# Kernel tuning notes

Hardware: AMD Instinct MI355X
Metric: run time of the kernel (lower is better)

The kernel has to match this reference:

```python
import jax, jax.numpy as jnp
import numpy as np

N, E = 20000, 320000
IN_F, EF, H, C = 2, 1, 128, 2
BN_S = 1.0 / float(np.sqrt(1.0 + 1e-5))  # eval-mode BatchNorm1d with running mean 0, var 1


def _gated_gcn_conv(h, e, src, dst, p, act, residual):
    # DGL GatedGCNConv: e' = C e + D h_src + E h_dst;
    # h' = A h + sum_{in-edges} sigmoid(e') * B h_src / (sum sigmoid(e') + 1e-6)
    Aw, Ab, Bw, Bb, Cw, Cb, Dw, Db, Ew, Eb, bhg, bhb, beg, beb = p
    h_in, e_in = h, e
    Ah = h @ Aw + Ab
    Bh = h @ Bw + Bb
    Dh = h @ Dw + Db
    Eh = h @ Ew + Eb
    e2 = e @ Cw + Cb + Dh[src] + Eh[dst]          # [E, H]
    sig = jax.nn.sigmoid(e2)
    num = jax.ops.segment_sum(sig * Bh[src], dst, num_segments=N)  # [N, H]
    den = jax.ops.segment_sum(sig, dst, num_segments=N)            # [N, H]
    h2 = Ah + num / (den + 1e-6)
    # BatchNorm (eval): (x - 0)/sqrt(1 + eps) * gamma + beta
    h2 = bhg * (h2 * BN_S) + bhb
    e2 = beg * (e2 * BN_S) + beb
    h2, e2 = act(h2), act(e2)
    if residual:
        h2 = h2 + h_in
        e2 = e2 + e_in
    return h2, e2


def _forward(node_feats, edge_feats, src, dst, P):
    (a0_w, a0_b, b0_w, b0_b, c0_w, c0_b, d0_w, d0_b, e0_w, e0_b,
     bnh0_g, bnh0_b, bne0_g, bne0_b,
     aL_w, aL_b, bL_w, bL_b, cL_w, cL_b, dL_w, dL_b, eL_w, eL_b,
     bnhL_g, bnhL_b, bneL_g, bneL_b,
     mlp_w1, mlp_b1, mlp_w2, mlp_b2) = P
    h, e = node_feats, edge_feats
    # layer 0: elu inside conv, residual off (2->128, 1->128)
    p0 = (a0_w, a0_b, b0_w, b0_b, c0_w, c0_b, d0_w, d0_b, e0_w, e0_b,
          bnh0_g, bnh0_b, bne0_g, bne0_b)
    h, e = _gated_gcn_conv(h, e, src, dst, p0, jax.nn.elu, residual=False)
    h = jax.nn.leaky_relu(h)
    e = jax.nn.leaky_relu(e)
    # layers 1..2: leaky_relu inside conv, residual on (128->128)
    for l in range(2):
        pl = (aL_w[l], aL_b[l], bL_w[l], bL_b[l], cL_w[l], cL_b[l],
              dL_w[l], dL_b[l], eL_w[l], eL_b[l],
              bnhL_g[l], bnhL_b[l], bneL_g[l], bneL_b[l])
        h, e = _gated_gcn_conv(h, e, src, dst, pl, jax.nn.leaky_relu, residual=True)
        h = jax.nn.leaky_relu(h)
        e = jax.nn.leaky_relu(e)
    # edge classifier: gather endpoints, concat with edge feats, MLP
    edge_repr = jnp.concatenate([h[src], h[dst], e], axis=1)  # [E, 3H]
    hid = jax.nn.relu(edge_repr @ mlp_w1 + mlp_b1)
    return hid @ mlp_w2 + mlp_b2                               # [E, C]


PARAM_NAMES = ["a0_w", "a0_b", "b0_w", "b0_b", "c0_w", "c0_b", "d0_w", "d0_b",
               "e0_w", "e0_b", "bnh0_g", "bnh0_b", "bne0_g", "bne0_b",
               "aL_w", "aL_b", "bL_w", "bL_b", "cL_w", "cL_b", "dL_w", "dL_b",
               "eL_w", "eL_b", "bnhL_g", "bnhL_b", "bneL_g", "bneL_b",
               "mlp_w1", "mlp_b1", "mlp_w2", "mlp_b2"]


def setup_inputs() -> dict:
    key = jax.random.key(0)
    ks = iter(jax.random.split(key, 64))
    nrm = lambda shp: jax.random.normal(next(ks), shp, dtype=jnp.float32) * 0.05
    inp = {}
    inp["node_feats"] = jax.random.normal(next(ks), (N, IN_F), dtype=jnp.float32)
    inp["edge_feats"] = jax.random.normal(next(ks), (E, EF), dtype=jnp.float32)
    inp["src"] = jax.random.randint(next(ks), (E,), 0, N, dtype=jnp.int32)
    inp["dst"] = jax.random.randint(next(ks), (E,), 0, N, dtype=jnp.int32)
    # layer 0 linears (A,B,D,E: in->H; C: edge->H), biases zero-init like common practice
    for nm, din in [("a0", IN_F), ("b0", IN_F), ("c0", EF), ("d0", IN_F), ("e0", IN_F)]:
        inp[nm + "_w"] = nrm((din, H))
        inp[nm + "_b"] = nrm((H,))
    inp["bnh0_g"] = jnp.ones((H,), jnp.float32)
    inp["bnh0_b"] = jnp.zeros((H,), jnp.float32)
    inp["bne0_g"] = jnp.ones((H,), jnp.float32)
    inp["bne0_b"] = jnp.zeros((H,), jnp.float32)
    # layers 1..2 stacked
    for nm in ["aL", "bL", "cL", "dL", "eL"]:
        inp[nm + "_w"] = nrm((2, H, H))
        inp[nm + "_b"] = nrm((2, H))
    inp["bnhL_g"] = jnp.ones((2, H), jnp.float32)
    inp["bnhL_b"] = jnp.zeros((2, H), jnp.float32)
    inp["bneL_g"] = jnp.ones((2, H), jnp.float32)
    inp["bneL_b"] = jnp.zeros((2, H), jnp.float32)
    # edge MLP
    inp["mlp_w1"] = nrm((3 * H, H))
    inp["mlp_b1"] = nrm((H,))
    inp["mlp_w2"] = nrm((H, C))
    inp["mlp_b2"] = nrm((C,))
    return inp


def reference(node_feats, edge_feats, src, dst,
              a0_w, a0_b, b0_w, b0_b, c0_w, c0_b, d0_w, d0_b, e0_w, e0_b,
              bnh0_g, bnh0_b, bne0_g, bne0_b,
              aL_w, aL_b, bL_w, bL_b, cL_w, cL_b, dL_w, dL_b, eL_w, eL_b,
              bnhL_g, bnhL_b, bneL_g, bneL_b,
              mlp_w1, mlp_b1, mlp_w2, mlp_b2):
    P = (a0_w, a0_b, b0_w, b0_b, c0_w, c0_b, d0_w, d0_b, e0_w, e0_b,
         bnh0_g, bnh0_b, bne0_g, bne0_b,
         aL_w, aL_b, bL_w, bL_b, cL_w, cL_b, dL_w, dL_b, eL_w, eL_b,
         bnhL_g, bnhL_b, bneL_g, bneL_b,
         mlp_w1, mlp_b1, mlp_w2, mlp_b2)
    return _forward(node_feats, edge_feats, src, dst, P)
```

## Files before the change

### kernel.cpp

```cpp
#include <hip/hip_runtime.h>
#include <hip/hip_bf16.h>
#include <math.h>

#define NN 20000
#define NE 320000
#define H 128
#define NH (NN * H)

typedef short bf16x8 __attribute__((ext_vector_type(8)));
typedef float f32x4 __attribute__((ext_vector_type(4)));
typedef unsigned short u16x8 __attribute__((ext_vector_type(8)));

__device__ __forceinline__ float lrelu(float x) { return x > 0.f ? x : 0.01f * x; }
__device__ __forceinline__ float eluf(float x)  { return x > 0.f ? x : expm1f(x); }
__device__ __forceinline__ float sigf(float x)  { return 1.f / (1.f + __expf(-x)); }
__device__ __forceinline__ unsigned short f2b(float x) {
    __hip_bfloat16 h = __float2bfloat16(x);
    return *reinterpret_cast<unsigned short*>(&h);
}
__device__ __forceinline__ float b2f(unsigned short u) {
    __hip_bfloat16 h = *reinterpret_cast<__hip_bfloat16*>(&u);
    return __bfloat162float(h);
}
#define BN_S 0.99999500003749973f

struct PackPtrs { const float* w[13]; };
__global__ __launch_bounds__(256) void k_pack(PackPtrs p, unsigned short* __restrict__ dst) {
    int gid = blockIdx.x * 256 + threadIdx.x;
    int m = gid >> 11;
    int r = gid & 2047;
    int t = r >> 8, kk = (r >> 6) & 3, lane = r & 63;
    const float* W = p.w[m];
    int col = t * 16 + (lane & 15);
    int krow = kk * 32 + (lane >> 4) * 8;
    unsigned short* o = dst + (size_t)m * 16384 + (size_t)r * 8;
#pragma unroll
    for (int j = 0; j < 8; ++j) o[j] = f2b(W[(krow + j) * H + col]);
}

__global__ __launch_bounds__(256) void k_deg(const int* __restrict__ dst, int* __restrict__ deg) {
    int e = blockIdx.x * 256 + threadIdx.x;
    if (e < NE) atomicAdd(&deg[dst[e]], 1);
}

__global__ __launch_bounds__(256) void k_scan(const int* __restrict__ deg,
                                              int* __restrict__ off, int* __restrict__ cursor) {
    __shared__ int sums[256];
    const int t = threadIdx.x;
    const int per = (NN + 255) / 256;
    const int base = t * per;
    int s = 0;
    for (int i = 0; i < per; ++i) { int idx = base + i; if (idx < NN) s += deg[idx]; }
    sums[t] = s;
    __syncthreads();
    for (int d = 1; d < 256; d <<= 1) {
        int v = (t >= d) ? sums[t - d] : 0;
        __syncthreads();
        sums[t] += v;
        __syncthreads();
    }
    int run = (t == 0) ? 0 : sums[t - 1];
    for (int i = 0; i < per; ++i) {
        int idx = base + i;
        if (idx < NN) { off[idx] = run; cursor[idx] = run; run += deg[idx]; }
    }
}

__global__ __launch_bounds__(256) void k_fill(const int* __restrict__ dst,
                                              int* __restrict__ cursor, int* __restrict__ csr) {
    int e = blockIdx.x * 256 + threadIdx.x;
    if (e < NE) {
        int pos = atomicAdd(&cursor[dst[e]], 1);
        csr[pos] = e;
    }
}

__global__ __launch_bounds__(256) void k_seqs(const int* __restrict__ csr,
                                              const int* __restrict__ src,
                                              const int* __restrict__ dst,
                                              const float* __restrict__ ef,
                                              int* __restrict__ srcseq,
                                              int* __restrict__ dstseq,
                                              float* __restrict__ efseq) {
    int pos = blockIdx.x * 256 + threadIdx.x;
    if (pos < NE) {
        int eid = csr[pos];
        srcseq[pos] = src[eid];
        dstseq[pos] = dst[eid];
        efseq[pos]  = ef[eid];
    }
}

__global__ __launch_bounds__(256) void k_nodelin0(
        const float* __restrict__ nf,
        const float* __restrict__ wa, const float* __restrict__ ba,
        const float* __restrict__ wb, const float* __restrict__ bb,
        const float* __restrict__ wd, const float* __restrict__ bd,
        const float* __restrict__ we, const float* __restrict__ be,
        float* __restrict__ lin) {
    int idx = blockIdx.x * 256 + threadIdx.x;
    int n = idx >> 7, c = idx & 127;
    float x0 = nf[n * 2], x1 = nf[n * 2 + 1];
    lin[0 * NH + idx] = fmaf(x0, wa[c], fmaf(x1, wa[128 + c], ba[c]));
    lin[1 * NH + idx] = fmaf(x0, wb[c], fmaf(x1, wb[128 + c], bb[c]));
    lin[2 * NH + idx] = fmaf(x0, wd[c], fmaf(x1, wd[128 + c], bd[c]));
    lin[3 * NH + idx] = fmaf(x0, we[c], fmaf(x1, we[128 + c], be[c]));
}

__global__ __launch_bounds__(256) void k_edge0(
        const float* __restrict__ efseq,
        const float* __restrict__ cw, const float* __restrict__ cb,
        const int* __restrict__ srcseq, const int* __restrict__ dstseq,
        const float* __restrict__ lin,
        const float* __restrict__ g, const float* __restrict__ bt,
        unsigned short* __restrict__ ebuf) {
    const int tid = threadIdx.x;
    const int pos = blockIdx.x * 8 + (tid >> 5);
    const int c0 = (tid & 31) * 4;
    const int s = srcseq[pos], d = dstseq[pos];
    const float ev = efseq[pos];
    const float4 cw4 = *(const float4*)(cw + c0);
    const float4 cb4 = *(const float4*)(cb + c0);
    const float4 Dh  = *(const float4*)(lin + 2 * NH + (size_t)s * H + c0);
    const float4 Eh  = *(const float4*)(lin + 3 * NH + (size_t)d * H + c0);
    const float4 g4  = *(const float4*)(g + c0);
    const float4 bt4 = *(const float4*)(bt + c0);
    float e2[4] = { fmaf(ev, cw4.x, cb4.x) + Dh.x + Eh.x,
                    fmaf(ev, cw4.y, cb4.y) + Dh.y + Eh.y,
                    fmaf(ev, cw4.z, cb4.z) + Dh.z + Eh.z,
                    fmaf(ev, cw4.w, cb4.w) + Dh.w + Eh.w };
    const float gg[4] = { g4.x, g4.y, g4.z, g4.w };
    const float bb[4] = { bt4.x, bt4.y, bt4.z, bt4.w };
    ushort4 u;
    u.x = f2b(lrelu(eluf(fmaf(gg[0], e2[0] * BN_S, bb[0]))));
    u.y = f2b(lrelu(eluf(fmaf(gg[1], e2[1] * BN_S, bb[1]))));
    u.z = f2b(lrelu(eluf(fmaf(gg[2], e2[2] * BN_S, bb[2]))));
    u.w = f2b(lrelu(eluf(fmaf(gg[3], e2[3] * BN_S, bb[3]))));
    *(ushort4*)(ebuf + (size_t)pos * H + c0) = u;
}

__global__ __launch_bounds__(256) void k_agg0(
        const int* __restrict__ off, const int* __restrict__ deg,
        const int* __restrict__ srcseq, const float* __restrict__ efseq,
        const float* __restrict__ cw, const float* __restrict__ cb,
        const float* __restrict__ lin,
        const float* __restrict__ g, const float* __restrict__ bt,
        float* __restrict__ hout, unsigned short* __restrict__ hbout) {
    const int tid = threadIdx.x;
    const int n = blockIdx.x * 2 + (tid >> 7);
    const int c = tid & 127;
    const int base = off[n], dg = deg[n];
    float num = 0.f, den = 0.f;
    const float Ehn = lin[3 * NH + (size_t)n * H + c];
    const float cwc = cw[c], cbc = cb[c];
    int i = 0;
    for (; i + 4 <= dg; i += 4) {
        int s0 = srcseq[base + i],     s1 = srcseq[base + i + 1];
        int s2 = srcseq[base + i + 2], s3 = srcseq[base + i + 3];
        float x0 = fmaf(efseq[base + i],     cwc, cbc) + lin[2 * NH + (size_t)s0 * H + c] + Ehn;
        float x1 = fmaf(efseq[base + i + 1], cwc, cbc) + lin[2 * NH + (size_t)s1 * H + c] + Ehn;
        float x2 = fmaf(efseq[base + i + 2], cwc, cbc) + lin[2 * NH + (size_t)s2 * H + c] + Ehn;
        float x3 = fmaf(efseq[base + i + 3], cwc, cbc) + lin[2 * NH + (size_t)s3 * H + c] + Ehn;
        float g0 = sigf(x0), g1 = sigf(x1), g2 = sigf(x2), g3 = sigf(x3);
        num = fmaf(g0, lin[1 * NH + (size_t)s0 * H + c], num); den += g0;
        num = fmaf(g1, lin[1 * NH + (size_t)s1 * H + c], num); den += g1;
        num = fmaf(g2, lin[1 * NH + (size_t)s2 * H + c], num); den += g2;
        num = fmaf(g3, lin[1 * NH + (size_t)s3 * H + c], num); den += g3;
    }
    for (; i < dg; ++i) {
        int sa = srcseq[base + i];
        float xa = fmaf(efseq[base + i], cwc, cbc) + lin[2 * NH + (size_t)sa * H + c] + Ehn;
        float ga = sigf(xa);
        num = fmaf(ga, lin[1 * NH + (size_t)sa * H + c], num); den += ga;
    }
    float h2 = lin[(size_t)n * H + c] + num / (den + 1e-6f);
    h2 = fmaf(g[c], h2 * BN_S, bt[c]);
    h2 = eluf(h2);
    float r = lrelu(h2);
    hout[(size_t)n * H + c] = r;
    hbout[(size_t)n * H + c] = f2b(r);
}

__global__ __launch_bounds__(256) void k_agg(
        const int* __restrict__ off, const int* __restrict__ deg,
        const int* __restrict__ srcseq,
        const unsigned short* __restrict__ e2seq,
        const float* __restrict__ lin,
        const float* __restrict__ g, const float* __restrict__ bt,
        const float* __restrict__ hin, float* __restrict__ hout,
        unsigned short* __restrict__ hbout) {
    const int tid = threadIdx.x;
    const int n = blockIdx.x * 2 + (tid >> 7);
    const int c = tid & 127;
    const int base = off[n], dg = deg[n];
    float num = 0.f, den = 0.f;
    int i = 0;
    for (; i + 4 <= dg; i += 4) {
        int s0 = srcseq[base + i],     s1 = srcseq[base + i + 1];
        int s2 = srcseq[base + i + 2], s3 = srcseq[base + i + 3];
        float x0 = b2f(e2seq[(size_t)(base + i) * H + c]);
        float x1 = b2f(e2seq[(size_t)(base + i + 1) * H + c]);
        float x2 = b2f(e2seq[(size_t)(base + i + 2) * H + c]);
        float x3 = b2f(e2seq[(size_t)(base + i + 3) * H + c]);
        float g0 = sigf(x0), g1 = sigf(x1), g2 = sigf(x2), g3 = sigf(x3);
        num = fmaf(g0, lin[1 * NH + (size_t)s0 * H + c], num); den += g0;
        num = fmaf(g1, lin[1 * NH + (size_t)s1 * H + c], num); den += g1;
        num = fmaf(g2, lin[1 * NH + (size_t)s2 * H + c], num); den += g2;
        num = fmaf(g3, lin[1 * NH + (size_t)s3 * H + c], num); den += g3;
    }
    for (; i < dg; ++i) {
        int sa = srcseq[base + i];
        float xa = b2f(e2seq[(size_t)(base + i) * H + c]);
        float ga = sigf(xa);
        num = fmaf(ga, lin[1 * NH + (size_t)sa * H + c], num); den += ga;
    }
    float h2 = lin[(size_t)n * H + c] + num / (den + 1e-6f);
    h2 = fmaf(g[c], h2 * BN_S, bt[c]);
    h2 = lrelu(h2);
    h2 += hin[(size_t)n * H + c];
    float r = lrelu(h2);
    hout[(size_t)n * H + c] = r;
    hbout[(size_t)n * H + c] = f2b(r);
}

__global__ __launch_bounds__(256) void k_nodegemm(
        const unsigned short* __restrict__ hb,
        const unsigned short* __restrict__ wpack,
        const float* __restrict__ ba, const float* __restrict__ bb,
        const float* __restrict__ bd, const float* __restrict__ be,
        float* __restrict__ lin) {
    __shared__ __align__(16) unsigned short AT[64][136];
    const int tid = threadIdx.x;
    const int nbase = blockIdx.x * 64;
    const int which = blockIdx.y;
    const unsigned short* Wp = wpack + (size_t)which * 16384;
    const float* B = which == 0 ? ba : which == 1 ? bb : which == 2 ? bd : be;
#pragma unroll
    for (int rep = 0; rep < 4; ++rep) {
        int flat = (rep * 256 + tid) * 8;
        int r = flat >> 7, k0 = flat & 127;
        int n = nbase + r;
        u16x8 v = {};
        if (n < NN) v = *(const u16x8*)(hb + (size_t)n * H + k0);
        *(u16x8*)(&AT[r][k0]) = v;
    }
    __syncthreads();
    const int lane = tid & 63, wave = tid >> 6;
    const int lrow = lane & 15, quad = lane >> 4;
    f32x4 acc[8] = {};
#pragma unroll
    for (int kk = 0; kk < 4; ++kk) {
        bf16x8 af = *(const bf16x8*)(&AT[wave * 16 + lrow][kk * 32 + quad * 8]);
#pragma unroll
        for (int t = 0; t < 8; ++t) {
            bf16x8 bfv = *(const bf16x8*)(Wp + ((t * 4 + kk) * 64 + lane) * 8);
            acc[t] = __builtin_amdgcn_mfma_f32_16x16x32_bf16(af, bfv, acc[t], 0, 0, 0);
        }
    }
#pragma unroll
    for (int t = 0; t < 8; ++t) {
        int col = t * 16 + lrow;
        float bv = B[col];
#pragma unroll
        for (int reg = 0; reg < 4; ++reg) {
            int n = nbase + wave * 16 + quad * 4 + reg;
            if (n < NN)
                lin[(size_t)which * NH + (size_t)n * H + col] = acc[t][reg] + bv;
        }
    }
}

__global__ __launch_bounds__(256) void k_pgemm(
        const unsigned short* __restrict__ hb,
        const unsigned short* __restrict__ w1p,
        const float* __restrict__ b1,
        float* __restrict__ P) {
    __shared__ __align__(16) unsigned short AT[64][136];
    const int tid = threadIdx.x;
    const int nbase = blockIdx.x * 64;
    const int y = blockIdx.y;
    const unsigned short* Wp = w1p + (size_t)y * 16384;
#pragma unroll
    for (int rep = 0; rep < 4; ++rep) {
        int flat = (rep * 256 + tid) * 8;
        int r = flat >> 7, k0 = flat & 127;
        int n = nbase + r;
        u16x8 v = {};
        if (n < NN) v = *(const u16x8*)(hb + (size_t)n * H + k0);
        *(u16x8*)(&AT[r][k0]) = v;
    }
    __syncthreads();
    const int lane = tid & 63, wave = tid >> 6;
    const int lrow = lane & 15, quad = lane >> 4;
    f32x4 acc[8] = {};
#pragma unroll
    for (int kk = 0; kk < 4; ++kk) {
        bf16x8 af = *(const bf16x8*)(&AT[wave * 16 + lrow][kk * 32 + quad * 8]);
#pragma unroll
        for (int t = 0; t < 8; ++t) {
            bf16x8 bfv = *(const bf16x8*)(Wp + ((t * 4 + kk) * 64 + lane) * 8);
            acc[t] = __builtin_amdgcn_mfma_f32_16x16x32_bf16(af, bfv, acc[t], 0, 0, 0);
        }
    }
#pragma unroll
    for (int t = 0; t < 8; ++t) {
        int col = t * 16 + lrow;
        float bv = (y == 0) ? b1[col] : 0.f;
#pragma unroll
        for (int reg = 0; reg < 4; ++reg) {
            int n = nbase + wave * 16 + quad * 4 + reg;
            if (n < NN)
                P[(size_t)y * NH + (size_t)n * H + col] = acc[t][reg] + bv;
        }
    }
}

__global__ __launch_bounds__(256) void k_edgegemm(
        unsigned short* __restrict__ ebuf,
        unsigned short* __restrict__ e2seq,
        const unsigned short* __restrict__ Wp,
        const float* __restrict__ cb,
        const int* __restrict__ srcseq, const int* __restrict__ dstseq,
        const float* __restrict__ lin,
        const float* __restrict__ g, const float* __restrict__ bt) {
    __shared__ __align__(16) unsigned short AT[64][136];
    const int tid = threadIdx.x;
    const int ebase = blockIdx.x * 64;
#pragma unroll
    for (int rep = 0; rep < 4; ++rep) {
        int flat = (rep * 256 + tid) * 8;
        int r = flat >> 7, k0 = flat & 127;
        *(u16x8*)(&AT[r][k0]) = *(const u16x8*)(ebuf + (size_t)(ebase + r) * H + k0);
    }
    __syncthreads();
    const int lane = tid & 63, wave = tid >> 6;
    const int lrow = lane & 15, quad = lane >> 4;
    f32x4 acc[8] = {};
#pragma unroll
    for (int kk = 0; kk < 4; ++kk) {
        bf16x8 af = *(const bf16x8*)(&AT[wave * 16 + lrow][kk * 32 + quad * 8]);
#pragma unroll
        for (int t = 0; t < 8; ++t) {
            bf16x8 bfv = *(const bf16x8*)(Wp + ((t * 4 + kk) * 64 + lane) * 8);
            acc[t] = __builtin_amdgcn_mfma_f32_16x16x32_bf16(af, bfv, acc[t], 0, 0, 0);
        }
    }
    const int r0 = ebase + wave * 16 + quad * 4;
    const int rr0 = wave * 16 + quad * 4;
    int sv[4], dv[4];
#pragma unroll
    for (int reg = 0; reg < 4; ++reg) {
        sv[reg] = srcseq[r0 + reg];
        dv[reg] = dstseq[r0 + reg];
    }
#pragma unroll
    for (int t = 0; t < 8; ++t) {
        int col = t * 16 + lrow;
        float cbv = cb[col], gv = g[col], btv = bt[col];
#pragma unroll
        for (int reg = 0; reg < 4; ++reg) {
            float Dh = lin[2 * NH + (size_t)sv[reg] * H + col];
            float Eh = lin[3 * NH + (size_t)dv[reg] * H + col];
            float e2 = acc[t][reg] + cbv + Dh + Eh;
            e2seq[(size_t)(r0 + reg) * H + col] = f2b(e2);
            float tt = lrelu(fmaf(gv, e2 * BN_S, btv));
            float ein = b2f(AT[rr0 + reg][col]);
            ebuf[(size_t)(r0 + reg) * H + col] = f2b(lrelu(tt + ein));
        }
    }
}

__global__ __launch_bounds__(256) void k_mlp2(
        const unsigned short* __restrict__ ebuf,
        const float* __restrict__ P,
        const int* __restrict__ csr,
        const int* __restrict__ srcseq, const int* __restrict__ dstseq,
        const unsigned short* __restrict__ w1p2,
        const float* __restrict__ w2, const float* __restrict__ b2,
        float* __restrict__ out) {
    __shared__ __align__(16) unsigned short AT[64][136];
    const int tid = threadIdx.x;
    const int ebase = blockIdx.x * 64;
#pragma unroll
    for (int rep = 0; rep < 4; ++rep) {
        int flat = (rep * 256 + tid) * 8;
        int r = flat >> 7, k0 = flat & 127;
        *(u16x8*)(&AT[r][k0]) = *(const u16x8*)(ebuf + (size_t)(ebase + r) * H + k0);
    }
    __syncthreads();
    const int lane = tid & 63, wave = tid >> 6;
    const int lrow = lane & 15, quad = lane >> 4;
    f32x4 acc[8] = {};
#pragma unroll
    for (int kk = 0; kk < 4; ++kk) {
        bf16x8 af = *(const bf16x8*)(&AT[wave * 16 + lrow][kk * 32 + quad * 8]);
#pragma unroll
        for (int t = 0; t < 8; ++t) {
            bf16x8 bfv = *(const bf16x8*)(w1p2 + ((t * 4 + kk) * 64 + lane) * 8);
            acc[t] = __builtin_amdgcn_mfma_f32_16x16x32_bf16(af, bfv, acc[t], 0, 0, 0);
        }
    }
    const int e0 = ebase + wave * 16 + quad * 4;
    const float b20 = b2[0], b21 = b2[1];
#pragma unroll
    for (int reg = 0; reg < 4; ++reg) {
        const int e = e0 + reg;
        const int s = srcseq[e], d = dstseq[e];
        float p1v[8], p2v[8];
#pragma unroll
        for (int t = 0; t < 8; ++t) {
            int col = t * 16 + lrow;
            p1v[t] = P[(size_t)s * H + col];
            p2v[t] = P[(size_t)NH + (size_t)d * H + col];
        }
        float p0 = 0.f, p1 = 0.f;
#pragma unroll
        for (int t = 0; t < 8; ++t) {
            int col = t * 16 + lrow;
            float hv = fmaxf(acc[t][reg] + p1v[t] + p2v[t], 0.f);
            p0 = fmaf(hv, w2[col * 2], p0);
            p1 = fmaf(hv, w2[col * 2 + 1], p1);
        }
#pragma unroll
        for (int off = 8; off; off >>= 1) {
            p0 += __shfl_xor(p0, off, 16);
            p1 += __shfl_xor(p1, off, 16);
        }
        if (lrow == 0) {
            int eid = csr[e];
            out[eid * 2]     = p0 + b20;
            out[eid * 2 + 1] = p1 + b21;
        }
    }
}

extern "C" void kernel_launch(void* const* d_in, const int* in_sizes, int n_in,
                              void* d_out, int out_size, void* d_ws, size_t ws_size,
                              hipStream_t stream) {
    const float* nf  = (const float*)d_in[0];
    const float* ef  = (const float*)d_in[1];
    const int*   src = (const int*)d_in[2];
    const int*   dst = (const int*)d_in[3];
    const float *a0w = (const float*)d_in[4],  *a0b = (const float*)d_in[5];
    const float *b0w = (const float*)d_in[6],  *b0b = (const float*)d_in[7];
    const float *c0w = (const float*)d_in[8],  *c0b = (const float*)d_in[9];
    const float *d0w = (const float*)d_in[10], *d0b = (const float*)d_in[11];
    const float *e0w = (const float*)d_in[12], *e0b = (const float*)d_in[13];
    const float *bnh0g = (const float*)d_in[14], *bnh0b = (const float*)d_in[15];
    const float *bne0g = (const float*)d_in[16], *bne0b = (const float*)d_in[17];
    const float *aLw = (const float*)d_in[18], *aLb = (const float*)d_in[19];
    const float *bLw = (const float*)d_in[20], *bLb = (const float*)d_in[21];
    const float *cLw = (const float*)d_in[22], *cLb = (const float*)d_in[23];
    const float *dLw = (const float*)d_in[24], *dLb = (const float*)d_in[25];
    const float *eLw = (const float*)d_in[26], *eLb = (const float*)d_in[27];
    const float *bnhLg = (const float*)d_in[28], *bnhLb = (const float*)d_in[29];
    const float *bneLg = (const float*)d_in[30], *bneLb = (const float*)d_in[31];
    const float *w1 = (const float*)d_in[32], *b1 = (const float*)d_in[33];
    const float *w2 = (const float*)d_in[34], *b2 = (const float*)d_in[35];
    float* out = (float*)d_out;

    char* ws = (char*)d_ws;
    unsigned short* ebuf  = (unsigned short*)ws;
    unsigned short* e2seq = ebuf + (size_t)NE * H;
    float* lin = (float*)(e2seq + (size_t)NE * H);
    float* h0  = lin + 4ull * NH;
    float* h1  = h0 + NH;
    unsigned short* hb0 = (unsigned short*)(h1 + NH);
    unsigned short* hb1 = hb0 + NH;
    int* deg    = (int*)(hb1 + NH);
    int* off    = deg + NN;
    int* cursor = off + NN;
    int* csr    = cursor + NN;
    int* srcseq = csr + NE;
    int* dstseq = srcseq + NE;
    float* efseq = (float*)(dstseq + NE);
    unsigned short* wpack = (unsigned short*)(efseq + NE);
    float* P = (float*)e2seq;

    PackPtrs pp;
    const size_t HH = (size_t)H * H;
    for (int l = 0; l < 2; ++l) {
        pp.w[l * 5 + 0] = aLw + l * HH;
        pp.w[l * 5 + 1] = bLw + l * HH;
        pp.w[l * 5 + 2] = dLw + l * HH;
        pp.w[l * 5 + 3] = eLw + l * HH;
        pp.w[l * 5 + 4] = cLw + l * HH;
    }
    pp.w[10] = w1; pp.w[11] = w1 + HH; pp.w[12] = w1 + 2 * HH;
    k_pack<<<104, 256, 0, stream>>>(pp, wpack);

    hipMemsetAsync(deg, 0, NN * sizeof(int), stream);
    k_deg<<<(NE + 255) / 256, 256, 0, stream>>>(dst, deg);
    k_scan<<<1, 256, 0, stream>>>(deg, off, cursor);
    k_fill<<<(NE + 255) / 256, 256, 0, stream>>>(dst, cursor, csr);
    k_seqs<<<(NE + 255) / 256, 256, 0, stream>>>(csr, src, dst, ef, srcseq, dstseq, efseq);

    k_nodelin0<<<NN * H / 256, 256, 0, stream>>>(nf, a0w, a0b, b0w, b0b, d0w, d0b, e0w, e0b, lin);
    k_edge0<<<NE / 8, 256, 0, stream>>>(efseq, c0w, c0b, srcseq, dstseq, lin,
                                        bne0g, bne0b, ebuf);
    k_agg0<<<NN / 2, 256, 0, stream>>>(off, deg, srcseq, efseq, c0w, c0b,
                                       lin, bnh0g, bnh0b, h0, hb0);

    for (int l = 0; l < 2; ++l) {
        const float* hin = (l == 0) ? h0 : h1;
        float* hout      = (l == 0) ? h1 : h0;
        const unsigned short* hbin = (l == 0) ? hb0 : hb1;
        unsigned short* hbout      = (l == 0) ? hb1 : hb0;
        k_nodegemm<<<dim3(313, 4), 256, 0, stream>>>(hbin,
            wpack + (size_t)l * 5 * 16384,
            aLb + l * H, bLb + l * H, dLb + l * H, eLb + l * H, lin);
        k_edgegemm<<<NE / 64, 256, 0, stream>>>(ebuf, e2seq,
                                                wpack + (size_t)(l * 5 + 4) * 16384,
                                                cLb + l * H, srcseq, dstseq, lin,
                                                bneLg + l * H, bneLb + l * H);
        k_agg<<<NN / 2, 256, 0, stream>>>(off, deg, srcseq, e2seq,
                                          lin, bnhLg + l * H, bnhLb + l * H,
                                          hin, hout, hbout);
    }

    k_pgemm<<<dim3(313, 2), 256, 0, stream>>>(hb0, wpack + 10ull * 16384, b1, P);
    k_mlp2<<<NE / 64, 256, 0, stream>>>(ebuf, P, csr, srcseq, dstseq,
                                        wpack + 12ull * 16384, w2, b2, out);

    (void)in_sizes; (void)n_in; (void)out_size; (void)ws_size;
}
```

Baseline: 666.5 us.

## Fuse gated aggregation into edge GEMM via atomics and store node projections in bf16

The sigmoid gating and numerator/denominator accumulation move into the edge GEMM epilogue. Each tile run-length-merges edges sharing a destination (edges are dst-sorted) and adds the partial sums with float atomics into an interleaved num/den buffer. This removes the e2seq round trip and the separate per-node gather-aggregation kernel, replacing it with a light elementwise node-update kernel. Separately, the B/D/E node projections and the MLP P matrix are now stored as bf16 instead of fp32, halving gather traffic. The cost is atomic contention, an extra memset per layer, reduced precision, and nondeterministic summation order.

```diff
diff --git a/kernel.cpp b/kernel.cpp
--- a/kernel.cpp
+++ b/kernel.cpp
@@ -97,21 +97,22 @@
         const float* __restrict__ wb, const float* __restrict__ bb,
         const float* __restrict__ wd, const float* __restrict__ bd,
         const float* __restrict__ we, const float* __restrict__ be,
-        float* __restrict__ lin) {
+        float* __restrict__ lin0, unsigned short* __restrict__ linB,
+        unsigned short* __restrict__ linD, unsigned short* __restrict__ linE) {
     int idx = blockIdx.x * 256 + threadIdx.x;
     int n = idx >> 7, c = idx & 127;
     float x0 = nf[n * 2], x1 = nf[n * 2 + 1];
-    lin[0 * NH + idx] = fmaf(x0, wa[c], fmaf(x1, wa[128 + c], ba[c]));
-    lin[1 * NH + idx] = fmaf(x0, wb[c], fmaf(x1, wb[128 + c], bb[c]));
-    lin[2 * NH + idx] = fmaf(x0, wd[c], fmaf(x1, wd[128 + c], bd[c]));
-    lin[3 * NH + idx] = fmaf(x0, we[c], fmaf(x1, we[128 + c], be[c]));
+    lin0[idx] = fmaf(x0, wa[c], fmaf(x1, wa[128 + c], ba[c]));
+    linB[idx] = f2b(fmaf(x0, wb[c], fmaf(x1, wb[128 + c], bb[c])));
+    linD[idx] = f2b(fmaf(x0, wd[c], fmaf(x1, wd[128 + c], bd[c])));
+    linE[idx] = f2b(fmaf(x0, we[c], fmaf(x1, we[128 + c], be[c])));
 }
 
 __global__ __launch_bounds__(256) void k_edge0(
         const float* __restrict__ efseq,
         const float* __restrict__ cw, const float* __restrict__ cb,
         const int* __restrict__ srcseq, const int* __restrict__ dstseq,
-        const float* __restrict__ lin,
+        const unsigned short* __restrict__ linD, const unsigned short* __restrict__ linE,
         const float* __restrict__ g, const float* __restrict__ bt,
         unsigned short* __restrict__ ebuf) {
     const int tid = threadIdx.x;
@@ -121,14 +122,14 @@
     const float ev = efseq[pos];
     const float4 cw4 = *(const float4*)(cw + c0);
     const float4 cb4 = *(const float4*)(cb + c0);
-    const float4 Dh  = *(const float4*)(lin + 2 * NH + (size_t)s * H + c0);
-    const float4 Eh  = *(const float4*)(lin + 3 * NH + (size_t)d * H + c0);
+    const ushort4 Dh = *(const ushort4*)(linD + (size_t)s * H + c0);
+    const ushort4 Eh = *(const ushort4*)(linE + (size_t)d * H + c0);
     const float4 g4  = *(const float4*)(g + c0);
     const float4 bt4 = *(const float4*)(bt + c0);
-    float e2[4] = { fmaf(ev, cw4.x, cb4.x) + Dh.x + Eh.x,
-                    fmaf(ev, cw4.y, cb4.y) + Dh.y + Eh.y,
-                    fmaf(ev, cw4.z, cb4.z) + Dh.z + Eh.z,
-                    fmaf(ev, cw4.w, cb4.w) + Dh.w + Eh.w };
+    float e2[4] = { fmaf(ev, cw4.x, cb4.x) + b2f(Dh.x) + b2f(Eh.x),
+                    fmaf(ev, cw4.y, cb4.y) + b2f(Dh.y) + b2f(Eh.y),
+                    fmaf(ev, cw4.z, cb4.z) + b2f(Dh.z) + b2f(Eh.z),
+                    fmaf(ev, cw4.w, cb4.w) + b2f(Dh.w) + b2f(Eh.w) };
     const float gg[4] = { g4.x, g4.y, g4.z, g4.w };
     const float bb[4] = { bt4.x, bt4.y, bt4.z, bt4.w };
     ushort4 u;
@@ -143,7 +144,8 @@
         const int* __restrict__ off, const int* __restrict__ deg,
         const int* __restrict__ srcseq, const float* __restrict__ efseq,
         const float* __restrict__ cw, const float* __restrict__ cb,
-        const float* __restrict__ lin,
+        const float* __restrict__ lin0, const unsigned short* __restrict__ linB,
+        const unsigned short* __restrict__ linD, const unsigned short* __restrict__ linE,
         const float* __restrict__ g, const float* __restrict__ bt,
         float* __restrict__ hout, unsigned short* __restrict__ hbout) {
     const int tid = threadIdx.x;
@@ -151,29 +153,29 @@
     const int c = tid & 127;
     const int base = off[n], dg = deg[n];
     float num = 0.f, den = 0.f;
-    const float Ehn = lin[3 * NH + (size_t)n * H + c];
+    const float Ehn = b2f(linE[(size_t)n * H + c]);
     const float cwc = cw[c], cbc = cb[c];
     int i = 0;
     for (; i + 4 <= dg; i += 4) {
         int s0 = srcseq[base + i],     s1 = srcseq[base + i + 1];
         int s2 = srcseq[base + i + 2], s3 = srcseq[base + i + 3];
-        float x0 = fmaf(efseq[base + i],     cwc, cbc) + lin[2 * NH + (size_t)s0 * H + c] + Ehn;
-        float x1 = fmaf(efseq[base + i + 1], cwc, cbc) + lin[2 * NH + (size_t)s1 * H + c] + Ehn;
-        float x2 = fmaf(efseq[base + i + 2], cwc, cbc) + lin[2 * NH + (size_t)s2 * H + c] + Ehn;
-        float x3 = fmaf(efseq[base + i + 3], cwc, cbc) + lin[2 * NH + (size_t)s3 * H + c] + Ehn;
+        float x0 = fmaf(efseq[base + i],     cwc, cbc) + b2f(linD[(size_t)s0 * H + c]) + Ehn;
+        float x1 = fmaf(efseq[base + i + 1], cwc, cbc) + b2f(linD[(size_t)s1 * H + c]) + Ehn;
+        float x2 = fmaf(efseq[base + i + 2], cwc, cbc) + b2f(linD[(size_t)s2 * H + c]) + Ehn;
+        float x3 = fmaf(efseq[base + i + 3], cwc, cbc) + b2f(linD[(size_t)s3 * H + c]) + Ehn;
         float g0 = sigf(x0), g1 = sigf(x1), g2 = sigf(x2), g3 = sigf(x3);
-        num = fmaf(g0, lin[1 * NH + (size_t)s0 * H + c], num); den += g0;
-        num = fmaf(g1, lin[1 * NH + (size_t)s1 * H + c], num); den += g1;
-        num = fmaf(g2, lin[1 * NH + (size_t)s2 * H + c], num); den += g2;
-        num = fmaf(g3, lin[1 * NH + (size_t)s3 * H + c], num); den += g3;
+        num = fmaf(g0, b2f(linB[(size_t)s0 * H + c]), num); den += g0;
+        num = fmaf(g1, b2f(linB[(size_t)s1 * H + c]), num); den += g1;
+        num = fmaf(g2, b2f(linB[(size_t)s2 * H + c]), num); den += g2;
+        num = fmaf(g3, b2f(linB[(size_t)s3 * H + c]), num); den += g3;
     }
     for (; i < dg; ++i) {
         int sa = srcseq[base + i];
-        float xa = fmaf(efseq[base + i], cwc, cbc) + lin[2 * NH + (size_t)sa * H + c] + Ehn;
+        float xa = fmaf(efseq[base + i], cwc, cbc) + b2f(linD[(size_t)sa * H + c]) + Ehn;
         float ga = sigf(xa);
-        num = fmaf(ga, lin[1 * NH + (size_t)sa * H + c], num); den += ga;
-    }
-    float h2 = lin[(size_t)n * H + c] + num / (den + 1e-6f);
+        num = fmaf(ga, b2f(linB[(size_t)sa * H + c]), num); den += ga;
+    }
+    float h2 = lin0[(size_t)n * H + c] + num / (den + 1e-6f);
     h2 = fmaf(g[c], h2 * BN_S, bt[c]);
     h2 = eluf(h2);
     float r = lrelu(h2);
@@ -181,46 +183,39 @@
     hbout[(size_t)n * H + c] = f2b(r);
 }
 
-__global__ __launch_bounds__(256) void k_agg(
-        const int* __restrict__ off, const int* __restrict__ deg,
-        const int* __restrict__ srcseq,
-        const unsigned short* __restrict__ e2seq,
-        const float* __restrict__ lin,
+__global__ __launch_bounds__(256) void k_nodeupd(
+        const float* __restrict__ lin0, const float* __restrict__ numden,
         const float* __restrict__ g, const float* __restrict__ bt,
         const float* __restrict__ hin, float* __restrict__ hout,
         unsigned short* __restrict__ hbout) {
-    const int tid = threadIdx.x;
-    const int n = blockIdx.x * 2 + (tid >> 7);
-    const int c = tid & 127;
-    const int base = off[n], dg = deg[n];
-    float num = 0.f, den = 0.f;
-    int i = 0;
-    for (; i + 4 <= dg; i += 4) {
-        int s0 = srcseq[base + i],     s1 = srcseq[base + i + 1];
-        int s2 = srcseq[base + i + 2], s3 = srcseq[base + i + 3];
-        float x0 = b2f(e2seq[(size_t)(base + i) * H + c]);
-        float x1 = b2f(e2seq[(size_t)(base + i + 1) * H + c]);
-        float x2 = b2f(e2seq[(size_t)(base + i + 2) * H + c]);
-        float x3 = b2f(e2seq[(size_t)(base + i + 3) * H + c]);
-        float g0 = sigf(x0), g1 = sigf(x1), g2 = sigf(x2), g3 = sigf(x3);
-        num = fmaf(g0, lin[1 * NH + (size_t)s0 * H + c], num); den += g0;
-        num = fmaf(g1, lin[1 * NH + (size_t)s1 * H + c], num); den += g1;
-        num = fmaf(g2, lin[1 * NH + (size_t)s2 * H + c], num); den += g2;
-        num = fmaf(g3, lin[1 * NH + (size_t)s3 * H + c], num); den += g3;
-    }
-    for (; i < dg; ++i) {
-        int sa = srcseq[base + i];
-        float xa = b2f(e2seq[(size_t)(base + i) * H + c]);
-        float ga = sigf(xa);
-        num = fmaf(ga, lin[1 * NH + (size_t)sa * H + c], num); den += ga;
-    }
-    float h2 = lin[(size_t)n * H + c] + num / (den + 1e-6f);
-    h2 = fmaf(g[c], h2 * BN_S, bt[c]);
-    h2 = lrelu(h2);
-    h2 += hin[(size_t)n * H + c];
-    float r = lrelu(h2);
-    hout[(size_t)n * H + c] = r;
-    hbout[(size_t)n * H + c] = f2b(r);
+    int idx = blockIdx.x * 256 + threadIdx.x;
+    int n = idx >> 5, c0 = (idx & 31) * 4;
+    int offh = n * H + c0;
+    const float4 Ah  = *(const float4*)(lin0 + offh);
+    const float4 nd0 = *(const float4*)(numden + (size_t)n * 256 + c0 * 2);
+    const float4 nd1 = *(const float4*)(numden + (size_t)n * 256 + c0 * 2 + 4);
+    const float4 g4 = *(const float4*)(g + c0);
+    const float4 b4 = *(const float4*)(bt + c0);
+    const float4 hi = *(const float4*)(hin + offh);
+    float a[4]  = { Ah.x, Ah.y, Ah.z, Ah.w };
+    float nu[4] = { nd0.x, nd0.z, nd1.x, nd1.z };
+    float de[4] = { nd0.y, nd0.w, nd1.y, nd1.w };
+    float gg[4] = { g4.x, g4.y, g4.z, g4.w };
+    float bb[4] = { b4.x, b4.y, b4.z, b4.w };
+    float r4[4] = { hi.x, hi.y, hi.z, hi.w };
+    float o[4];
+    ushort4 ub;
+#pragma unroll
+    for (int j = 0; j < 4; ++j) {
+        float h2 = a[j] + nu[j] / (de[j] + 1e-6f);
+        h2 = fmaf(gg[j], h2 * BN_S, bb[j]);
+        h2 = lrelu(h2);
+        h2 += r4[j];
+        o[j] = lrelu(h2);
+    }
+    ub.x = f2b(o[0]); ub.y = f2b(o[1]); ub.z = f2b(o[2]); ub.w = f2b(o[3]);
+    *(float4*)(hout + offh) = make_float4(o[0], o[1], o[2], o[3]);
+    *(ushort4*)(hbout + offh) = ub;
 }
 
 __global__ __launch_bounds__(256) void k_nodegemm(
@@ -228,7 +223,8 @@
         const unsigned short* __restrict__ wpack,
         const float* __restrict__ ba, const float* __restrict__ bb,
         const float* __restrict__ bd, const float* __restrict__ be,
-        float* __restrict__ lin) {
+        float* __restrict__ lin0, unsigned short* __restrict__ linB,
+        unsigned short* __restrict__ linD, unsigned short* __restrict__ linE) {
     __shared__ __align__(16) unsigned short AT[64][136];
     const int tid = threadIdx.x;
     const int nbase = blockIdx.x * 64;
@@ -257,6 +253,7 @@
             acc[t] = __builtin_amdgcn_mfma_f32_16x16x32_bf16(af, bfv, acc[t], 0, 0, 0);
         }
     }
+    unsigned short* linX = which == 1 ? linB : which == 2 ? linD : linE;
 #pragma unroll
     for (int t = 0; t < 8; ++t) {
         int col = t * 16 + lrow;
@@ -264,8 +261,11 @@
 #pragma unroll
         for (int reg = 0; reg < 4; ++reg) {
             int n = nbase + wave * 16 + quad * 4 + reg;
-            if (n < NN)
-                lin[(size_t)which * NH + (size_t)n * H + col] = acc[t][reg] + bv;
+            if (n < NN) {
+                float v = acc[t][reg] + bv;
+                if (which == 0) lin0[(size_t)n * H + col] = v;
+                else            linX[(size_t)n * H + col] = f2b(v);
+            }
         }
     }
 }
@@ -274,7 +274,7 @@
         const unsigned short* __restrict__ hb,
         const unsigned short* __restrict__ w1p,
         const float* __restrict__ b1,
-        float* __restrict__ P) {
+        unsigned short* __restrict__ P) {
     __shared__ __align__(16) unsigned short AT[64][136];
     const int tid = threadIdx.x;
     const int nbase = blockIdx.x * 64;
@@ -310,18 +310,20 @@
         for (int reg = 0; reg < 4; ++reg) {
             int n = nbase + wave * 16 + quad * 4 + reg;
             if (n < NN)
-                P[(size_t)y * NH + (size_t)n * H + col] = acc[t][reg] + bv;
+                P[(size_t)y * NH + (size_t)n * H + col] = f2b(acc[t][reg] + bv);
         }
     }
 }
 
 __global__ __launch_bounds__(256) void k_edgegemm(
         unsigned short* __restrict__ ebuf,
-        unsigned short* __restrict__ e2seq,
         const unsigned short* __restrict__ Wp,
         const float* __restrict__ cb,
         const int* __restrict__ srcseq, const int* __restrict__ dstseq,
-        const float* __restrict__ lin,
+        const unsigned short* __restrict__ linB,
+        const unsigned short* __restrict__ linD,
+        const unsigned short* __restrict__ linE,
+        float* __restrict__ numden,
         const float* __restrict__ g, const float* __restrict__ bt) {
     __shared__ __align__(16) unsigned short AT[64][136];
     const int tid = threadIdx.x;
@@ -357,22 +359,38 @@
     for (int t = 0; t < 8; ++t) {
         int col = t * 16 + lrow;
         float cbv = cb[col], gv = g[col], btv = bt[col];
+        float sg[4], bh[4];
 #pragma unroll
         for (int reg = 0; reg < 4; ++reg) {
-            float Dh = lin[2 * NH + (size_t)sv[reg] * H + col];
-            float Eh = lin[3 * NH + (size_t)dv[reg] * H + col];
+            float Dh = b2f(linD[(size_t)sv[reg] * H + col]);
+            float Eh = b2f(linE[(size_t)dv[reg] * H + col]);
+            bh[reg]  = b2f(linB[(size_t)sv[reg] * H + col]);
             float e2 = acc[t][reg] + cbv + Dh + Eh;
-            e2seq[(size_t)(r0 + reg) * H + col] = f2b(e2);
+            sg[reg] = sigf(e2);
             float tt = lrelu(fmaf(gv, e2 * BN_S, btv));
             float ein = b2f(AT[rr0 + reg][col]);
             ebuf[(size_t)(r0 + reg) * H + col] = f2b(lrelu(tt + ein));
         }
+        float np = 0.f, dp = 0.f;
+        int cur = dv[0];
+#pragma unroll
+        for (int reg = 0; reg < 4; ++reg) {
+            if (dv[reg] != cur) {
+                atomicAdd(numden + (size_t)cur * 256 + col * 2,     np);
+                atomicAdd(numden + (size_t)cur * 256 + col * 2 + 1, dp);
+                np = 0.f; dp = 0.f; cur = dv[reg];
+            }
+            np = fmaf(sg[reg], bh[reg], np);
+            dp += sg[reg];
+        }
+        atomicAdd(numden + (size_t)cur * 256 + col * 2,     np);
+        atomicAdd(numden + (size_t)cur * 256 + col * 2 + 1, dp);
     }
 }
 
 __global__ __launch_bounds__(256) void k_mlp2(
         const unsigned short* __restrict__ ebuf,
-        const float* __restrict__ P,
+        const unsigned short* __restrict__ P,
         const int* __restrict__ csr,
         const int* __restrict__ srcseq, const int* __restrict__ dstseq,
         const unsigned short* __restrict__ w1p2,
@@ -410,8 +428,8 @@
 #pragma unroll
         for (int t = 0; t < 8; ++t) {
             int col = t * 16 + lrow;
-            p1v[t] = P[(size_t)s * H + col];
-            p2v[t] = P[(size_t)NH + (size_t)d * H + col];
+            p1v[t] = b2f(P[(size_t)s * H + col]);
+            p2v[t] = b2f(P[(size_t)NH + (size_t)d * H + col]);
         }
         float p0 = 0.f, p1 = 0.f;
 #pragma unroll
@@ -460,10 +478,13 @@
     float* out = (float*)d_out;
 
     char* ws = (char*)d_ws;
-    unsigned short* ebuf  = (unsigned short*)ws;
-    unsigned short* e2seq = ebuf + (size_t)NE * H;
-    float* lin = (float*)(e2seq + (size_t)NE * H);
-    float* h0  = lin + 4ull * NH;
+    unsigned short* ebuf = (unsigned short*)ws;
+    float* lin0 = (float*)(ebuf + (size_t)NE * H);
+    unsigned short* linB = (unsigned short*)(lin0 + NH);
+    unsigned short* linD = linB + NH;
+    unsigned short* linE = linD + NH;
+    float* numden = (float*)(linE + NH);
+    float* h0  = numden + (size_t)NN * 256;
     float* h1  = h0 + NH;
     unsigned short* hb0 = (unsigned short*)(h1 + NH);
     unsigned short* hb1 = hb0 + NH;
@@ -475,7 +496,7 @@
     int* dstseq = srcseq + NE;
     float* efseq = (float*)(dstseq + NE);
     unsigned short* wpack = (unsigned short*)(efseq + NE);
-    float* P = (float*)e2seq;
+    unsigned short* P = wpack + 13ull * 16384;
 
     PackPtrs pp;
     const size_t HH = (size_t)H * H;
@@ -495,11 +516,12 @@
     k_fill<<<(NE + 255) / 256, 256, 0, stream>>>(dst, cursor, csr);
     k_seqs<<<(NE + 255) / 256, 256, 0, stream>>>(csr, src, dst, ef, srcseq, dstseq, efseq);
 
-    k_nodelin0<<<NN * H / 256, 256, 0, stream>>>(nf, a0w, a0b, b0w, b0b, d0w, d0b, e0w, e0b, lin);
-    k_edge0<<<NE / 8, 256, 0, stream>>>(efseq, c0w, c0b, srcseq, dstseq, lin,
+    k_nodelin0<<<NN * H / 256, 256, 0, stream>>>(nf, a0w, a0b, b0w, b0b, d0w, d0b,
+                                                 e0w, e0b, lin0, linB, linD, linE);
+    k_edge0<<<NE / 8, 256, 0, stream>>>(efseq, c0w, c0b, srcseq, dstseq, linD, linE,
                                         bne0g, bne0b, ebuf);
     k_agg0<<<NN / 2, 256, 0, stream>>>(off, deg, srcseq, efseq, c0w, c0b,
-                                       lin, bnh0g, bnh0b, h0, hb0);
+                                       lin0, linB, linD, linE, bnh0g, bnh0b, h0, hb0);
 
     for (int l = 0; l < 2; ++l) {
         const float* hin = (l == 0) ? h0 : h1;
@@ -508,14 +530,17 @@
         unsigned short* hbout      = (l == 0) ? hb1 : hb0;
         k_nodegemm<<<dim3(313, 4), 256, 0, stream>>>(hbin,
             wpack + (size_t)l * 5 * 16384,
-            aLb + l * H, bLb + l * H, dLb + l * H, eLb + l * H, lin);
-        k_edgegemm<<<NE / 64, 256, 0, stream>>>(ebuf, e2seq,
+            aLb + l * H, bLb + l * H, dLb + l * H, eLb + l * H,
+            lin0, linB, linD, linE);
+        hipMemsetAsync(numden, 0, (size_t)NN * 256 * sizeof(float), stream);
+        k_edgegemm<<<NE / 64, 256, 0, stream>>>(ebuf,
                                                 wpack + (size_t)(l * 5 + 4) * 16384,
-                                                cLb + l * H, srcseq, dstseq, lin,
+                                                cLb + l * H, srcseq, dstseq,
+                                                linB, linD, linE, numden,
                                                 bneLg + l * H, bneLb + l * H);
-        k_agg<<<NN / 2, 256, 0, stream>>>(off, deg, srcseq, e2seq,
-                                          lin, bnhLg + l * H, bnhLb + l * H,
-                                          hin, hout, hbout);
+        k_nodeupd<<<NN * 32 / 256, 256, 0, stream>>>(lin0, numden,
+                                                     bnhLg + l * H, bnhLb + l * H,
+                                                     hin, hout, hbout);
     }
 
     k_pgemm<<<dim3(313, 2), 256, 0, stream>>>(hb0, wpack + 10ull * 16384, b1, P);
```

New measurement: 974.6 us. 46.2% more time.
